# Kernel tuning notes

Hardware: AMD Instinct MI355X
Metric: run time of the kernel (lower is better)

Reference implementation:

```python
import jax, jax.numpy as jnp
import numpy as np

NUM_JOINTS = 32
N_E = 1024
E_DIM = 128
BETA = 0.25
HID = 256
CHAINS = [[0,1,2,3,4,5],[0,6,7,8,9,10],[0,11,12,13,14,15],
          [12,16,17,18,19,20,21,22,23],[12,24,25,26,27,28,29,30,31]]


def setup_inputs() -> dict:
    key = jax.random.key(0)
    ks = jax.random.split(key, 8)
    B, T = 64, 128
    z = jax.random.normal(ks[0], (B, T, NUM_JOINTS, E_DIM), jnp.float32)
    # xavier_uniform for embeddings: bound = sqrt(6/(n_e+e_dim))
    eb = float(np.sqrt(6.0 / (N_E + E_DIM)))
    emb = jax.random.uniform(ks[1], (NUM_JOINTS, N_E, E_DIM), jnp.float32, -eb, eb)
    # torch Linear default init: U(-1/sqrt(fan_in), 1/sqrt(fan_in))
    b1b = float(1.0 / np.sqrt(2 * E_DIM))
    W1 = jax.random.uniform(ks[2], (2 * E_DIM, HID), jnp.float32, -b1b, b1b)
    b1 = jax.random.uniform(ks[3], (HID,), jnp.float32, -b1b, b1b)
    ln_g = jnp.ones((HID,), jnp.float32)
    ln_b = jnp.zeros((HID,), jnp.float32)
    b2b = float(1.0 / np.sqrt(HID))
    W2 = jax.random.uniform(ks[4], (HID, E_DIM), jnp.float32, -b2b, b2b)
    b2 = jax.random.uniform(ks[5], (E_DIM,), jnp.float32, -b2b, b2b)
    return {"z": z, "emb": emb, "W1": W1, "b1": b1, "ln_g": ln_g,
            "ln_b": ln_b, "W2": W2, "b2": b2}


def _layernorm(x, g, b, eps=1e-5):
    m = jnp.mean(x, axis=-1, keepdims=True)
    v = jnp.mean((x - m) ** 2, axis=-1, keepdims=True)
    return (x - m) * jax.lax.rsqrt(v + eps) * g + b


def _mlp(x, W1, b1, ln_g, ln_b, W2, b2):
    h = x @ W1 + b1
    h = jax.nn.relu(_layernorm(h, ln_g, ln_b))
    return h @ W2 + b2


def _quantize_joint(h, E):
    # h: [B,T,C], E: [n_e,C]. argmin of euclidean dist == argmin of -2 h.E^T + |E|^2
    B, T, C = h.shape
    hf = h.reshape(-1, C)
    d = -2.0 * (hf @ E.T) + jnp.sum(E * E, axis=1)  # [B*T, n_e]
    idx = jnp.argmin(d, axis=1)
    e = E[idx].reshape(B, T, C)  # one-hot @ E == gather
    sg = jax.lax.stop_gradient
    loss = jnp.mean((sg(e) - h) ** 2) + BETA * jnp.mean((e - sg(h)) ** 2)
    q = h + sg(e - h)  # straight-through
    return q, e, idx.reshape(B, T), loss


def reference(z, emb, W1, b1, ln_g, ln_b, W2, b2):
    B, T, V, C = z.shape
    sg = jax.lax.stop_gradient
    stored_q, stored_e, stored_idx = {}, {}, {}
    total = jnp.zeros((), z.dtype)
    for chain in CHAINS:
        parent_e = None
        for i, j in enumerate(chain):
            if j not in stored_q:  # single-pass per joint
                zj = z[:, :, j, :]
                h = _mlp(jnp.concatenate([parent_e, zj], -1), W1, b1, ln_g, ln_b, W2, b2) if i > 0 else zj
                q, e, idx, loss = _quantize_joint(h, emb[j])
                stored_q[j], stored_e[j], stored_idx[j] = q, e, idx
                total = total + loss
            parent_e = sg(stored_e[j])
    z_q = jnp.stack([stored_q[v] for v in range(V)], axis=2)      # [B,T,V,C]
    indices = jnp.stack([stored_idx[v] for v in range(V)], axis=2)  # [B,T,V]
    return z_q, total / V, indices
```

## Files before the change

kernel.cpp:

```cpp
#include <hip/hip_runtime.h>

#define NJ 32
#define NE 1024
#define CD 128
#define HID 256
#define ROWS 8192

struct Lv { int nj; int j[5]; int p[5]; };

__global__ __launch_bounds__(256) void norms_kernel(const float* __restrict__ emb,
                                                    float* __restrict__ nrm) {
  int gid = blockIdx.x * 256 + threadIdx.x;
  int n = gid >> 2, l = gid & 3;
  const float* row = emb + (size_t)n * CD;
  float s = 0.f;
#pragma unroll
  for (int i = 0; i < 8; ++i) {
    float4 v = *(const float4*)&row[(l + 4 * i) * 4];
    s += v.x * v.x + v.y * v.y + v.z * v.z + v.w * v.w;
  }
  s += __shfl_xor(s, 1);
  s += __shfl_xor(s, 2);
  if (l == 0) nrm[n] = s;
}

template <int RB>
__global__ __launch_bounds__(256) void fused_level(
    const float* __restrict__ z, const float* __restrict__ emb,
    const float* __restrict__ W1, const float* __restrict__ b1,
    const float* __restrict__ lng, const float* __restrict__ lnb,
    const float* __restrict__ W2, const float* __restrict__ b2,
    const float* __restrict__ nrm,
    float* __restrict__ zq, float* __restrict__ idx_out,
    float* __restrict__ partials, Lv lv, int pbase) {
  constexpr int RPG = RB / 8;
  constexpr int R3  = RB / 16;
  constexpr int R4  = RB / 4;
  constexpr int HSP = RB + 4;
  constexpr int BPJ = ROWS / RB;
  constexpr int XS  = 256 * HSP;
  constexpr int HS  = 128 * HSP;
  constexpr int P4  = HS + 16 * 516 + 512;
  constexpr int SMEM = (XS > P4) ? XS : P4;

  __shared__ __align__(16) float smem[SMEM];
  __shared__ float wsum[4];
  float* xs  = smem;
  float* hs  = smem;
  float* as_ = smem + HS;
  float* es  = smem + HS;
  float* nsm = smem + HS + 16 * 516;

  const int tid = threadIdx.x;
  const int rg = tid >> 5, cg = tid & 31;
  const int u = cg & 15;
  const int qcA = (cg >> 4) * 128 + u * 4;
  const int qcB = qcA + 64;
  const int jl = blockIdx.x / BPJ;
  const int row0 = (blockIdx.x % BPJ) * RB;
  const int jj = lv.j[jl], pj = lv.p[jl];
  const size_t rstride = (size_t)NJ * CD;

  if (pj >= 0) {
    float acc1[RPG][8];
#pragma unroll
    for (int r = 0; r < RPG; ++r)
#pragma unroll
      for (int c = 0; c < 8; ++c) acc1[r][c] = 0.f;

#pragma unroll 1
    for (int ks = 0; ks < 8; ++ks) {
#pragma unroll
      for (int uu = 0; uu < RB / 32; ++uu) {
        int idx = uu * 256 + tid;
        int r = idx >> 3, kq = idx & 7;
        const float* src = (ks < 4)
            ? (zq + (size_t)(row0 + r) * rstride + (size_t)pj * CD + (ks * 32 + kq * 4))
            : (z  + (size_t)(row0 + r) * rstride + (size_t)jj * CD + (ks * 32 - 128 + kq * 4));
        float4 v = *(const float4*)src;
        xs[(ks * 32 + kq * 4 + 0) * HSP + r] = v.x;
        xs[(ks * 32 + kq * 4 + 1) * HSP + r] = v.y;
        xs[(ks * 32 + kq * 4 + 2) * HSP + r] = v.z;
        xs[(ks * 32 + kq * 4 + 3) * HSP + r] = v.w;
      }
    }
    __syncthreads();
#pragma unroll 4
    for (int kk = 0; kk < 256; ++kk) {
      float xr[RPG], wc[8];
      if constexpr (RPG >= 4) {
#pragma unroll
        for (int g = 0; g < RPG / 4; ++g)
          *(float4*)&xr[g * 4] = *(const float4*)&xs[kk * HSP + rg * RPG + g * 4];
      } else {
#pragma unroll
        for (int g = 0; g < RPG; ++g) xr[g] = xs[kk * HSP + rg * RPG + g];
      }
      *(float4*)&wc[0] = *(const float4*)&W1[(size_t)kk * HID + qcA];
      *(float4*)&wc[4] = *(const float4*)&W1[(size_t)kk * HID + qcB];
#pragma unroll
      for (int r = 0; r < RPG; ++r)
#pragma unroll
        for (int c = 0; c < 8; ++c)
          acc1[r][c] += xr[r] * wc[c];
    }

    {
      float bb[8], gg[8], be[8];
      *(float4*)&bb[0] = *(const float4*)&b1[qcA];
      *(float4*)&bb[4] = *(const float4*)&b1[qcB];
      *(float4*)&gg[0] = *(const float4*)&lng[qcA];
      *(float4*)&gg[4] = *(const float4*)&lng[qcB];
      *(float4*)&be[0] = *(const float4*)&lnb[qcA];
      *(float4*)&be[4] = *(const float4*)&lnb[qcB];
#pragma unroll
      for (int r = 0; r < RPG; ++r) {
        float s0 = 0.f, q0 = 0.f;
#pragma unroll
        for (int j = 0; j < 8; ++j) {
          float v = acc1[r][j] + bb[j];
          acc1[r][j] = v;
          s0 += v; q0 += v * v;
        }
        float si = __shfl_xor(s0, 16), qi = __shfl_xor(q0, 16);
        float s1 = si, q1 = qi;
#pragma unroll
        for (int j = 0; j < 8; ++j) {
          float v = acc1[r][j];
          s1 += v; q1 += v * v;
        }
#pragma unroll
        for (int m = 1; m < 16; m <<= 1) {
          s1 += __shfl_xor(s1, m); q1 += __shfl_xor(q1, m);
        }
        float s2 = __shfl_xor(s1, 16), q2 = __shfl_xor(q1, 16);
        float Sx = (cg & 16) ? s1 : s2;
        float Qx = (cg & 16) ? q1 : q2;
        float mu = Sx * (1.f / HID);
        float va = Qx * (1.f / HID) - mu * mu;
        float iv = 1.f / sqrtf(va + 1e-5f);
#pragma unroll
        for (int j = 0; j < 8; ++j) {
          float a = (acc1[r][j] - mu) * iv * gg[j] + be[j];
          acc1[r][j] = fmaxf(a, 0.f);
        }
      }
    }

    const int cc = tid & 15, rr = tid >> 4;
    const int qA = cc * 4, qB = qA + 64;
    float acc2[R3][8];
#pragma unroll
    for (int r = 0; r < R3; ++r)
#pragma unroll
      for (int c = 0; c < 8; ++c) acc2[r][c] = 0.f;

#pragma unroll 1
    for (int half = 0; half < 2; ++half) {
      __syncthreads();
      if ((cg >> 4) == half) {
#pragma unroll
        for (int j = 0; j < 8; ++j) {
          int kl = (j >> 2) * 64 + u * 4 + (j & 3);
#pragma unroll
          for (int g = 0; g < RPG; ++g)
            as_[kl * HSP + rg * RPG + g] = acc1[g][j];
        }
      }
      __syncthreads();
#pragma unroll 4
      for (int kk = 0; kk < 128; ++kk) {
        float ar[R3], wc2[8];
        if constexpr (R3 >= 4) {
#pragma unroll
          for (int g = 0; g < R3 / 4; ++g)
            *(float4*)&ar[g * 4] = *(const float4*)&as_[kk * HSP + rr * R3 + g * 4];
        } else {
#pragma unroll
          for (int g = 0; g < R3; ++g) ar[g] = as_[kk * HSP + rr * R3 + g];
        }
        *(float4*)&wc2[0] = *(const float4*)&W2[(size_t)(half * 128 + kk) * CD + qA];
        *(float4*)&wc2[4] = *(const float4*)&W2[(size_t)(half * 128 + kk) * CD + qB];
#pragma unroll
        for (int r = 0; r < R3; ++r)
#pragma unroll
          for (int c = 0; c < 8; ++c)
            acc2[r][c] += ar[r] * wc2[c];
      }
    }
    {
      float bbA[4], bbB[4];
      *(float4*)&bbA[0] = *(const float4*)&b2[qA];
      *(float4*)&bbB[0] = *(const float4*)&b2[qB];
#pragma unroll
      for (int c = 0; c < 8; ++c) {
        int col = (c < 4) ? (qA + c) : (qB + c - 4);
        float bb2 = (c < 4) ? bbA[c] : bbB[c - 4];
#pragma unroll
        for (int r = 0; r < R3; ++r)
          hs[col * HSP + rr * R3 + r] = acc2[r][c] + bb2;
      }
    }
  } else {
#pragma unroll
    for (int v = 0; v < RB / 8; ++v) {
      int idx = v * 256 + tid;
      int r = idx >> 5, c4 = idx & 31;
      float4 vz = *(const float4*)&z[(size_t)(row0 + r) * rstride + (size_t)jj * CD + c4 * 4];
      hs[(c4 * 4 + 0) * HSP + r] = vz.x;
      hs[(c4 * 4 + 1) * HSP + r] = vz.y;
      hs[(c4 * 4 + 2) * HSP + r] = vz.z;
      hs[(c4 * 4 + 3) * HSP + r] = vz.w;
    }
  }

  const int w4 = tid >> 6;
  const int l4 = tid & 63;
  float mnv[R4]; int mni[R4];
#pragma unroll
  for (int r = 0; r < R4; ++r) { mnv[r] = 3.402823e38f; mni[r] = 0; }
  const float* embJ = emb + (size_t)jj * NE * CD;
  const float* nrmJ = nrm + jj * NE;

#pragma unroll 1
  for (int p = 0; p < 2; ++p) {
    __syncthreads();
    if (tid < 128) {
      *(float4*)&nsm[tid * 4] = *(const float4*)&nrmJ[p * 512 + tid * 4];
    }
    float acc4[R4][8];
#pragma unroll
    for (int r = 0; r < R4; ++r)
#pragma unroll
      for (int c = 0; c < 8; ++c) acc4[r][c] = 0.f;

#pragma unroll 1
    for (int kc = 0; kc < 8; ++kc) {
#pragma unroll
      for (int v = 0; v < 8; ++v) {
        int idx = v * 256 + tid;
        int n = idx >> 2, kq = idx & 3;
        float4 ev = *(const float4*)&embJ[(size_t)(p * 512 + n) * CD + kc * 16 + kq * 4];
        es[(kq * 4 + 0) * 516 + n] = ev.x;
        es[(kq * 4 + 1) * 516 + n] = ev.y;
        es[(kq * 4 + 2) * 516 + n] = ev.z;
        es[(kq * 4 + 3) * 516 + n] = ev.w;
      }
      __syncthreads();
#pragma unroll 2
      for (int kk = 0; kk < 16; ++kk) {
        int c = kc * 16 + kk;
        float hr[R4], ec[8];
#pragma unroll
        for (int g = 0; g < R4 / 4; ++g)
          *(float4*)&hr[g * 4] = *(const float4*)&hs[c * HSP + w4 * R4 + g * 4];
        *(float4*)&ec[0] = *(const float4*)&es[kk * 516 + l4 * 4];
        *(float4*)&ec[4] = *(const float4*)&es[kk * 516 + 256 + l4 * 4];
#pragma unroll
        for (int r = 0; r < R4; ++r)
#pragma unroll
          for (int c2 = 0; c2 < 8; ++c2)
            acc4[r][c2] += hr[r] * ec[c2];
      }
      __syncthreads();
    }
#pragma unroll
    for (int r = 0; r < R4; ++r) {
#pragma unroll
      for (int q = 0; q < 2; ++q) {
#pragma unroll
        for (int j = 0; j < 4; ++j) {
          int nl = q * 256 + l4 * 4 + j;
          float d = nsm[nl] - 2.f * acc4[r][q * 4 + j];
          int n = p * 512 + nl;
          if (d < mnv[r]) { mnv[r] = d; mni[r] = n; }
        }
      }
    }
  }

#pragma unroll
  for (int r = 0; r < R4; ++r) {
    float mv = mnv[r]; int mi = mni[r];
#pragma unroll
    for (int m = 1; m < 64; m <<= 1) {
      float om = __shfl_xor(mv, m); int oi = __shfl_xor(mi, m);
      if (om < mv || (om == mv && oi < mi)) { mv = om; mi = oi; }
    }
    mnv[r] = mv; mni[r] = mi;
  }

  float lsum = 0.f;
#pragma unroll
  for (int r = 0; r < R4; ++r) {
    int row = w4 * R4 + r;
    int id = mni[r];
    const float* erow = embJ + (size_t)id * CD;
    float2 ev = *(const float2*)&erow[l4 * 2];
    float h0 = hs[(l4 * 2 + 0) * HSP + row];
    float h1 = hs[(l4 * 2 + 1) * HSP + row];
    float dx = ev.x - h0, dy = ev.y - h1;
    lsum += dx * dx + dy * dy;
    *(float2*)&zq[(size_t)(row0 + row) * rstride + (size_t)jj * CD + l4 * 2] = ev;
    if (l4 == r) idx_out[(size_t)(row0 + row) * NJ + jj] = (float)id;
  }
#pragma unroll
  for (int m = 1; m < 64; m <<= 1) lsum += __shfl_xor(lsum, m);
  if (l4 == 0) wsum[w4] = lsum;
  __syncthreads();
  if (tid == 0) partials[pbase + blockIdx.x] = wsum[0] + wsum[1] + wsum[2] + wsum[3];
}

__global__ __launch_bounds__(256) void loss_reduce(const float* __restrict__ p, int n,
                                                   float* __restrict__ out) {
  __shared__ float ws[4];
  float s = 0.f;
  for (int i = threadIdx.x; i < n; i += 256) s += p[i];
#pragma unroll
  for (int m = 1; m < 64; m <<= 1) s += __shfl_xor(s, m);
  if ((threadIdx.x & 63) == 0) ws[threadIdx.x >> 6] = s;
  __syncthreads();
  if (threadIdx.x == 0)
    out[0] = (ws[0] + ws[1] + ws[2] + ws[3]) * (1.25f / (1048576.f * 32.f));
}

extern "C" void kernel_launch(void* const* d_in, const int* in_sizes, int n_in,
                              void* d_out, int out_size, void* d_ws, size_t ws_size,
                              hipStream_t stream) {
  const float* z = (const float*)d_in[0];
  const float* emb = (const float*)d_in[1];
  const float* W1 = (const float*)d_in[2];
  const float* b1 = (const float*)d_in[3];
  const float* lng = (const float*)d_in[4];
  const float* lnb = (const float*)d_in[5];
  const float* W2 = (const float*)d_in[6];
  const float* b2 = (const float*)d_in[7];

  float* zq = (float*)d_out;
  float* loss = zq + (size_t)ROWS * NJ * CD;
  float* idxo = loss + 1;

  float* nrm = (float*)d_ws;
  float* partials = nrm + NJ * NE;

  norms_kernel<<<NJ * NE * 4 / 256, 256, 0, stream>>>(emb, nrm);

  static const Lv levels[11] = {
      {1, {0, 0, 0, 0, 0}, {-1, 0, 0, 0, 0}},
      {3, {1, 6, 11, 0, 0}, {0, 0, 0, 0, 0}},
      {3, {2, 7, 12, 0, 0}, {1, 6, 11, 0, 0}},
      {5, {3, 8, 13, 16, 24}, {2, 7, 12, 12, 12}},
      {5, {4, 9, 14, 17, 25}, {3, 8, 13, 16, 24}},
      {5, {5, 10, 15, 18, 26}, {4, 9, 14, 17, 25}},
      {2, {19, 27, 0, 0, 0}, {18, 26, 0, 0, 0}},
      {2, {20, 28, 0, 0, 0}, {19, 27, 0, 0, 0}},
      {2, {21, 29, 0, 0, 0}, {20, 28, 0, 0, 0}},
      {2, {22, 30, 0, 0, 0}, {21, 29, 0, 0, 0}},
      {2, {23, 31, 0, 0, 0}, {22, 30, 0, 0, 0}},
  };
  static const int rbs[11] = {16, 64, 64, 64, 64, 64, 32, 32, 32, 32, 32};

  int pbase = 0;
  for (int L = 0; L < 11; ++L) {
    int bpj = ROWS / rbs[L];
    int blocks = levels[L].nj * bpj;
    if (rbs[L] == 64) {
      fused_level<64><<<blocks, 256, 0, stream>>>(
          z, emb, W1, b1, lng, lnb, W2, b2, nrm, zq, idxo, partials, levels[L], pbase);
    } else if (rbs[L] == 32) {
      fused_level<32><<<blocks, 256, 0, stream>>>(
          z, emb, W1, b1, lng, lnb, W2, b2, nrm, zq, idxo, partials, levels[L], pbase);
    } else {
      fused_level<16><<<blocks, 256, 0, stream>>>(
          z, emb, W1, b1, lng, lnb, W2, b2, nrm, zq, idxo, partials, levels[L], pbase);
    }
    pbase += blocks;
  }
  loss_reduce<<<1, 256, 0, stream>>>(partials, pbase, loss);
}
```

Before: 1.955 ms.

## Prefetch codebook tiles into registers and shrink shared memory footprint

The codebook distance loop now processes 256 codes per pass instead of 512, and software-prefetches the next embedding chunk into registers while the current chunk is consumed from shared memory. The first MLP layer stages its input in two 128-wide halves, and the norms are read directly from global memory, which shrinks shared memory enough to allow more blocks per CU. The aim is to hide global load latency and raise occupancy, at the cost of more passes over the hidden tile, more barriers and more per-thread registers for the prefetch.

```diff
diff --git a/kernel.cpp b/kernel.cpp
--- a/kernel.cpp
+++ b/kernel.cpp
@@ -38,18 +38,14 @@
   constexpr int R4  = RB / 4;
   constexpr int HSP = RB + 4;
   constexpr int BPJ = ROWS / RB;
-  constexpr int XS  = 256 * HSP;
-  constexpr int HS  = 128 * HSP;
-  constexpr int P4  = HS + 16 * 516 + 512;
-  constexpr int SMEM = (XS > P4) ? XS : P4;
+  constexpr int SMEM = 128 * HSP + 16 * 260;
 
   __shared__ __align__(16) float smem[SMEM];
   __shared__ float wsum[4];
   float* xs  = smem;
+  float* as_ = smem;
   float* hs  = smem;
-  float* as_ = smem + HS;
-  float* es  = smem + HS;
-  float* nsm = smem + HS + 16 * 516;
+  float* es  = smem + 128 * HSP;
 
   const int tid = threadIdx.x;
   const int rg = tid >> 5, cg = tid & 31;
@@ -69,40 +65,45 @@
       for (int c = 0; c < 8; ++c) acc1[r][c] = 0.f;
 
 #pragma unroll 1
-    for (int ks = 0; ks < 8; ++ks) {
-#pragma unroll
-      for (int uu = 0; uu < RB / 32; ++uu) {
-        int idx = uu * 256 + tid;
-        int r = idx >> 3, kq = idx & 7;
-        const float* src = (ks < 4)
-            ? (zq + (size_t)(row0 + r) * rstride + (size_t)pj * CD + (ks * 32 + kq * 4))
-            : (z  + (size_t)(row0 + r) * rstride + (size_t)jj * CD + (ks * 32 - 128 + kq * 4));
-        float4 v = *(const float4*)src;
-        xs[(ks * 32 + kq * 4 + 0) * HSP + r] = v.x;
-        xs[(ks * 32 + kq * 4 + 1) * HSP + r] = v.y;
-        xs[(ks * 32 + kq * 4 + 2) * HSP + r] = v.z;
-        xs[(ks * 32 + kq * 4 + 3) * HSP + r] = v.w;
-      }
-    }
-    __syncthreads();
+    for (int ch = 0; ch < 2; ++ch) {
+      if (ch) __syncthreads();
+#pragma unroll
+      for (int v = 0; v < RB / 8; ++v) {
+        int idx = v * 256 + tid;
+        int kq = idx & 7;
+        int r = (idx >> 3) & (RB - 1);
+        int g32 = idx >> (3 + (RB == 64 ? 6 : (RB == 32 ? 5 : 4)));
+        const float* src = (ch == 0)
+            ? (zq + (size_t)(row0 + r) * rstride + (size_t)pj * CD + g32 * 32 + kq * 4)
+            : (z  + (size_t)(row0 + r) * rstride + (size_t)jj * CD + g32 * 32 + kq * 4);
+        float4 x4 = *(const float4*)src;
+        int kb = g32 * 32 + kq * 4;
+        xs[(kb + 0) * HSP + r] = x4.x;
+        xs[(kb + 1) * HSP + r] = x4.y;
+        xs[(kb + 2) * HSP + r] = x4.z;
+        xs[(kb + 3) * HSP + r] = x4.w;
+      }
+      __syncthreads();
 #pragma unroll 4
-    for (int kk = 0; kk < 256; ++kk) {
-      float xr[RPG], wc[8];
-      if constexpr (RPG >= 4) {
-#pragma unroll
-        for (int g = 0; g < RPG / 4; ++g)
-          *(float4*)&xr[g * 4] = *(const float4*)&xs[kk * HSP + rg * RPG + g * 4];
-      } else {
-#pragma unroll
-        for (int g = 0; g < RPG; ++g) xr[g] = xs[kk * HSP + rg * RPG + g];
-      }
-      *(float4*)&wc[0] = *(const float4*)&W1[(size_t)kk * HID + qcA];
-      *(float4*)&wc[4] = *(const float4*)&W1[(size_t)kk * HID + qcB];
-#pragma unroll
-      for (int r = 0; r < RPG; ++r)
-#pragma unroll
-        for (int c = 0; c < 8; ++c)
-          acc1[r][c] += xr[r] * wc[c];
+      for (int kk = 0; kk < 128; ++kk) {
+        float xr[RPG], wc[8];
+        const float* Wrow = &W1[(size_t)(ch * 128 + kk) * HID];
+        *(float4*)&wc[0] = *(const float4*)&Wrow[qcA];
+        *(float4*)&wc[4] = *(const float4*)&Wrow[qcB];
+        if constexpr (RPG >= 4) {
+#pragma unroll
+          for (int g = 0; g < RPG / 4; ++g)
+            *(float4*)&xr[g * 4] = *(const float4*)&xs[kk * HSP + rg * RPG + g * 4];
+        } else {
+#pragma unroll
+          for (int g = 0; g < RPG; ++g) xr[g] = xs[kk * HSP + rg * RPG + g];
+        }
+#pragma unroll
+        for (int r = 0; r < RPG; ++r)
+#pragma unroll
+          for (int c = 0; c < 8; ++c)
+            acc1[r][c] += xr[r] * wc[c];
+      }
     }
 
     {
@@ -170,7 +171,10 @@
       __syncthreads();
 #pragma unroll 4
       for (int kk = 0; kk < 128; ++kk) {
-        float ar[R3], wc2[8];
+        float ar[R3], w2[8];
+        const float* Wrow = &W2[(size_t)(half * 128 + kk) * CD];
+        *(float4*)&w2[0] = *(const float4*)&Wrow[qA];
+        *(float4*)&w2[4] = *(const float4*)&Wrow[qB];
         if constexpr (R3 >= 4) {
 #pragma unroll
           for (int g = 0; g < R3 / 4; ++g)
@@ -179,15 +183,14 @@
 #pragma unroll
           for (int g = 0; g < R3; ++g) ar[g] = as_[kk * HSP + rr * R3 + g];
         }
-        *(float4*)&wc2[0] = *(const float4*)&W2[(size_t)(half * 128 + kk) * CD + qA];
-        *(float4*)&wc2[4] = *(const float4*)&W2[(size_t)(half * 128 + kk) * CD + qB];
 #pragma unroll
         for (int r = 0; r < R3; ++r)
 #pragma unroll
           for (int c = 0; c < 8; ++c)
-            acc2[r][c] += ar[r] * wc2[c];
-      }
-    }
+            acc2[r][c] += ar[r] * w2[c];
+      }
+    }
+    __syncthreads();
     {
       float bbA[4], bbB[4];
       *(float4*)&bbA[0] = *(const float4*)&b2[qA];
@@ -216,68 +219,79 @@
 
   const int w4 = tid >> 6;
   const int l4 = tid & 63;
+  const int n0 = tid >> 2, kqe = tid & 3;
   float mnv[R4]; int mni[R4];
 #pragma unroll
   for (int r = 0; r < R4; ++r) { mnv[r] = 3.402823e38f; mni[r] = 0; }
   const float* embJ = emb + (size_t)jj * NE * CD;
   const float* nrmJ = nrm + jj * NE;
 
+  float4 pf0, pf1, pf2, pf3;
+#define LOADP(pp, kcc) { \
+    const float* bp = embJ + ((size_t)((pp) * 256 + n0)) * CD + (kcc) * 16 + kqe * 4; \
+    pf0 = *(const float4*)(bp); \
+    pf1 = *(const float4*)(bp + (size_t)64 * CD); \
+    pf2 = *(const float4*)(bp + (size_t)128 * CD); \
+    pf3 = *(const float4*)(bp + (size_t)192 * CD); }
+
+  LOADP(0, 0);
 #pragma unroll 1
-  for (int p = 0; p < 2; ++p) {
-    __syncthreads();
-    if (tid < 128) {
-      *(float4*)&nsm[tid * 4] = *(const float4*)&nrmJ[p * 512 + tid * 4];
-    }
-    float acc4[R4][8];
+  for (int p = 0; p < 4; ++p) {
+    float4 nr = *(const float4*)&nrmJ[p * 256 + l4 * 4];
+    float acc4[R4][4];
 #pragma unroll
     for (int r = 0; r < R4; ++r)
 #pragma unroll
-      for (int c = 0; c < 8; ++c) acc4[r][c] = 0.f;
+      for (int c = 0; c < 4; ++c) acc4[r][c] = 0.f;
 
 #pragma unroll 1
     for (int kc = 0; kc < 8; ++kc) {
-#pragma unroll
-      for (int v = 0; v < 8; ++v) {
-        int idx = v * 256 + tid;
-        int n = idx >> 2, kq = idx & 3;
-        float4 ev = *(const float4*)&embJ[(size_t)(p * 512 + n) * CD + kc * 16 + kq * 4];
-        es[(kq * 4 + 0) * 516 + n] = ev.x;
-        es[(kq * 4 + 1) * 516 + n] = ev.y;
-        es[(kq * 4 + 2) * 516 + n] = ev.z;
-        es[(kq * 4 + 3) * 516 + n] = ev.w;
-      }
-      __syncthreads();
-#pragma unroll 2
+      __syncthreads();
+      {
+        float* e0 = &es[(kqe * 4 + 0) * 260];
+        float* e1 = &es[(kqe * 4 + 1) * 260];
+        float* e2 = &es[(kqe * 4 + 2) * 260];
+        float* e3 = &es[(kqe * 4 + 3) * 260];
+        e0[n0]       = pf0.x; e1[n0]       = pf0.y; e2[n0]       = pf0.z; e3[n0]       = pf0.w;
+        e0[n0 + 64]  = pf1.x; e1[n0 + 64]  = pf1.y; e2[n0 + 64]  = pf1.z; e3[n0 + 64]  = pf1.w;
+        e0[n0 + 128] = pf2.x; e1[n0 + 128] = pf2.y; e2[n0 + 128] = pf2.z; e3[n0 + 128] = pf2.w;
+        e0[n0 + 192] = pf3.x; e1[n0 + 192] = pf3.y; e2[n0 + 192] = pf3.z; e3[n0 + 192] = pf3.w;
+      }
+      if (!(p == 3 && kc == 7)) {
+        int np = (kc == 7) ? p + 1 : p;
+        int nk = (kc == 7) ? 0 : kc + 1;
+        LOADP(np, nk);
+      }
+      __syncthreads();
+#pragma unroll 4
       for (int kk = 0; kk < 16; ++kk) {
         int c = kc * 16 + kk;
-        float hr[R4], ec[8];
+        float hr[R4], ec[4];
 #pragma unroll
         for (int g = 0; g < R4 / 4; ++g)
           *(float4*)&hr[g * 4] = *(const float4*)&hs[c * HSP + w4 * R4 + g * 4];
-        *(float4*)&ec[0] = *(const float4*)&es[kk * 516 + l4 * 4];
-        *(float4*)&ec[4] = *(const float4*)&es[kk * 516 + 256 + l4 * 4];
+        *(float4*)&ec[0] = *(const float4*)&es[kk * 260 + l4 * 4];
 #pragma unroll
         for (int r = 0; r < R4; ++r)
 #pragma unroll
-          for (int c2 = 0; c2 < 8; ++c2)
+          for (int c2 = 0; c2 < 4; ++c2)
             acc4[r][c2] += hr[r] * ec[c2];
       }
-      __syncthreads();
-    }
-#pragma unroll
-    for (int r = 0; r < R4; ++r) {
-#pragma unroll
-      for (int q = 0; q < 2; ++q) {
+    }
+    {
+      float nrr[4] = {nr.x, nr.y, nr.z, nr.w};
+#pragma unroll
+      for (int r = 0; r < R4; ++r) {
 #pragma unroll
         for (int j = 0; j < 4; ++j) {
-          int nl = q * 256 + l4 * 4 + j;
-          float d = nsm[nl] - 2.f * acc4[r][q * 4 + j];
-          int n = p * 512 + nl;
+          float d = nrr[j] - 2.f * acc4[r][j];
+          int n = p * 256 + l4 * 4 + j;
           if (d < mnv[r]) { mnv[r] = d; mni[r] = n; }
         }
       }
     }
   }
+#undef LOADP
 
 #pragma unroll
   for (int r = 0; r < R4; ++r) {
```

New measurement: 2.337 ms. 1.2x slower.
